# Optimization experiments

Measured on AMD Instinct MI355X. Metric: run time of the kernel, lower is better.

The kernel has to match this reference:

```python
import jax, jax.numpy as jnp
import numpy as np

H = 512        # hidden_dim
D_IN = 512     # input_dim
N_ACT = 16     # output_dim
DICT = 8192    # dict_len (episodic memory slots)
B = 4096       # batch
N_CYCLES = 10  # LCA iterations
DT_T = 0.6     # LCA dt/tau
EPS = 1e-8     # cosine-similarity eps


def setup_inputs() -> dict:
    key = jax.random.key(0)
    ks = jax.random.split(key, 12)
    NHT = 4 * H + 3  # (N_VSIG+1)*H + N_SSIG
    s = lambda i, shape, sc=1.0: jax.random.normal(ks[i], shape, jnp.float32) * sc
    return {
        "x_t": s(0, (1, B, D_IN)),
        "h_prev": s(1, (1, B, H), 0.1),
        "c_prev": s(2, (1, B, H), 0.1),
        "W_i2h": s(3, (NHT, D_IN), 1.0 / np.sqrt(D_IN)),
        "b_i2h": jnp.zeros((NHT,), jnp.float32),
        "W_h2h": s(4, (NHT, H), 1.0 / np.sqrt(H)),
        "b_h2h": jnp.zeros((NHT,), jnp.float32),
        "vals": s(5, (DICT, H), 0.1),  # episodic memory table
        "W_ih": s(6, (H, H), 1.0 / np.sqrt(H)),
        "b_ih": jnp.zeros((H,), jnp.float32),
        "W_actor": s(7, (N_ACT, H), 1.0 / np.sqrt(H)),
        "b_actor": jnp.zeros((N_ACT,), jnp.float32),
        "W_critic": s(8, (1, H), 1.0 / np.sqrt(H)),
        "b_critic": jnp.zeros((1,), jnp.float32),
        "mem_ptr": 0,
    }


def _lca(sim, leak, comp, w_input):
    # Leaky competing accumulator over memory slots; sim:[B,DICT], scalars:[B,1]
    ff = w_input * sim
    def step(V, _):
        inhib = comp * (jnp.sum(V, axis=-1, keepdims=True) - V)  # lateral inhibition (excl. self)
        V = jax.nn.relu(V + DT_T * (ff - leak * V - inhib))
        return V, None
    V, _ = jax.lax.scan(step, jnp.zeros_like(sim), None, length=N_CYCLES)
    return V


def reference(x_t, h_prev, c_prev, W_i2h, b_i2h, W_h2h, b_h2h, vals,
              W_ih, b_ih, W_actor, b_actor, W_critic, b_critic, mem_ptr):
    x, h, c = x_t[0], h_prev[0], c_prev[0]  # [B, dim]
    preact = x @ W_i2h.T + b_i2h + h @ W_h2h.T + b_h2h  # [B, 4H+3]
    gates = jax.nn.sigmoid(preact[:, :3 * H])
    f_t = gates[:, :H]
    o_t = gates[:, H:2 * H]
    i_t = gates[:, 2 * H:3 * H]
    inps = jax.nn.sigmoid(preact[:, 3 * H + 0])[:, None]  # input strength (gain=1)
    leak = jax.nn.sigmoid(preact[:, 3 * H + 1])[:, None]
    comp = jax.nn.sigmoid(preact[:, 3 * H + 2])[:, None]
    c_new = jnp.tanh(preact[:, 3 * H + 3:])
    c_t = c * f_t + i_t * c_new
    # --- recall: cosine similarity vs memory, then LCA competition ---
    qn = jnp.linalg.norm(c_t, axis=-1, keepdims=True)        # [B,1]
    mn = jnp.linalg.norm(vals, axis=-1, keepdims=True)       # [DICT,1]
    sim = (c_t @ vals.T) / jnp.maximum(qn * mn.T, EPS)       # [B,DICT]
    w = _lca(sim, leak, comp, inps)                          # [B,DICT]
    m_t = w @ vals                                           # [B,H]
    cm_t = c_t + m_t
    # --- encode: ring-buffer scatter write of cm_t into memory ---
    idx = (mem_ptr + jnp.arange(B)) % DICT
    new_vals = vals.at[idx].set(cm_t)
    h_t = o_t * jnp.tanh(cm_t)
    # --- A2C head ---
    a2c_h = jax.nn.relu(h_t @ W_ih.T + b_ih)
    pi = jax.nn.softmax(a2c_h @ W_actor.T + b_actor, axis=-1)
    value = a2c_h @ W_critic.T + b_critic
    return pi, value, h_t, cm_t, m_t, new_vals
```

## Files before the change

### kernel.cpp

```cpp
#include <hip/hip_runtime.h>
#include <hip/hip_fp16.h>
#include <math.h>

#define HH    512
#define DICT  8192
#define BATCH 4096
#define NCYC  10
#define DTT   0.6f

#define BM  128
#define BKT 64

using f16x8 = __attribute__((ext_vector_type(8))) _Float16;
using f32x4 = __attribute__((ext_vector_type(4))) float;

__device__ __forceinline__ float sigmoidf_(float x) { return 1.0f / (1.0f + __expf(-x)); }

__device__ __forceinline__ float waveReduceSum(float v) {
#pragma unroll
  for (int o = 1; o < 64; o <<= 1) v += __shfl_xor(v, o);
  return v;
}

__device__ __forceinline__ void gld16(const void* g, void* l) {
  __builtin_amdgcn_global_load_lds(
      (const __attribute__((address_space(1))) void*)g,
      (__attribute__((address_space(3))) void*)l, 16, 0, 0);
}

template<int N> __device__ __forceinline__ void vmwait() {
  if constexpr (N == 8)      asm volatile("s_waitcnt vmcnt(8)" ::: "memory");
  else if constexpr (N == 6) asm volatile("s_waitcnt vmcnt(6)" ::: "memory");
  else if constexpr (N == 2) asm volatile("s_waitcnt vmcnt(2)" ::: "memory");
  else                       asm volatile("s_waitcnt vmcnt(0)" ::: "memory");
  __builtin_amdgcn_sched_barrier(0);
}

__device__ __forceinline__ void blockbar() {
  asm volatile("" ::: "memory");
  __builtin_amdgcn_s_barrier();
  __builtin_amdgcn_sched_barrier(0);
}

template<int ROWS>
__device__ __forceinline__ void stage_tile(const __half* gbase, int ld, char* lds, int tid) {
  constexpr int ISS = ROWS * 8 / 256;
#pragma unroll
  for (int i = 0; i < ISS; ++i) {
    int cidx = i * 256 + tid;
    int row  = cidx >> 3;
    int slot = cidx & 7;
    int k4   = slot ^ (row & 7);
    gld16(gbase + (size_t)row * ld + k4 * 8, lds + cidx * 16);
  }
}

__device__ __forceinline__ f16x8 frag_ld(const char* lds, int row, int kchunk) {
  int slot = kchunk ^ (row & 7);
  return *(const f16x8*)(lds + row * 128 + slot * 16);
}

template<int FN>
__device__ __forceinline__ void tile_mfma(const char* As, const char* Bs,
                                          int lane, int wr, int wc, f32x4 (&acc)[4][FN]) {
  const int g = lane >> 4, r = lane & 15;
#pragma unroll
  for (int ks = 0; ks < 2; ++ks) {
    f16x8 af[4], bfr[FN];
#pragma unroll
    for (int i = 0; i < 4; ++i)
      af[i] = frag_ld(As, wr * 64 + i * 16 + r, ks * 4 + g);
#pragma unroll
    for (int j = 0; j < FN; ++j)
      bfr[j] = frag_ld(Bs, wc * (FN * 16) + j * 16 + r, ks * 4 + g);
#pragma unroll
    for (int i = 0; i < 4; ++i)
#pragma unroll
      for (int j = 0; j < FN; ++j)
        acc[i][j] = __builtin_amdgcn_mfma_f32_16x16x32_f16(af[i], bfr[j], acc[i][j], 0, 0, 0);
  }
}

template<int BN, int FN>
__device__ __forceinline__ void gemm_seg(const __half* A, int lda, const __half* B, int ldb,
                                         int m0, int n0, int K, char* lds, int tid,
                                         f32x4 (&acc)[4][FN]) {
  constexpr int ABYTES = BM * BKT * 2;
  constexpr int BBYTES = BN * BKT * 2;
  constexpr int BUF = ABYTES + BBYTES;
  constexpr int NL = (BM + BN) * 8 / 256;
  const int lane = tid & 63, wid = tid >> 6;
  const int wr = wid >> 1, wc = wid & 1;
  const int nt = K / BKT;
  const __half* Ab = A + (size_t)m0 * lda;
  const __half* Bb = B + (size_t)n0 * ldb;
  stage_tile<BM>(Ab, lda, lds, tid);
  stage_tile<BN>(Bb, ldb, lds + ABYTES, tid);
  int cur = 0;
  for (int t = 0; t < nt; ++t) {
    char* curb = lds + cur * BUF;
    if (t + 1 < nt) {
      char* nxt = lds + (cur ^ 1) * BUF;
      stage_tile<BM>(Ab + (t + 1) * BKT, lda, nxt, tid);
      stage_tile<BN>(Bb + (t + 1) * BKT, ldb, nxt + ABYTES, tid);
      vmwait<NL>();
    } else {
      vmwait<0>();
    }
    blockbar();
    tile_mfma<FN>(curb, curb + ABYTES, lane, wr, wc, acc);
    blockbar();
    cur ^= 1;
  }
}

__device__ __forceinline__ void zero_acc4(f32x4 (&a)[4][4]) {
  f32x4 z = {0.f, 0.f, 0.f, 0.f};
#pragma unroll
  for (int i = 0; i < 4; ++i)
#pragma unroll
    for (int j = 0; j < 4; ++j) a[i][j] = z;
}
__device__ __forceinline__ void zero_acc2(f32x4 (&a)[4][2]) {
  f32x4 z = {0.f, 0.f, 0.f, 0.f};
#pragma unroll
  for (int i = 0; i < 4; ++i)
#pragma unroll
    for (int j = 0; j < 2; ++j) a[i][j] = z;
}

__device__ __forceinline__ void stage_half(const __half* tilebase, int ld, char* ldstile,
                                           int h, int kcol, int tid) {
#pragma unroll
  for (int i = 0; i < 2; ++i) {
    int cidx = i * 512 + tid;
    int lrow = cidx >> 3;
    int slot = cidx & 7;
    int row  = h * 128 + lrow;
    int k4   = slot ^ (row & 7);
    gld16(tilebase + (size_t)row * ld + kcol + k4 * 8,
          ldstile + row * 128 + slot * 16);
  }
}

__device__ __forceinline__ f16x8 fragA8(const char* At, int fi, int wr, int ks, int lane) {
  int r = lane & 15, g = lane >> 4;
  int row = fi * 32 + wr * 16 + r;
  int slot = (ks * 4 + g) ^ (row & 7);
  return *(const f16x8*)(At + row * 128 + slot * 16);
}
__device__ __forceinline__ f16x8 fragB8(const char* Bt, int j, int wc, int ks, int lane) {
  int r = lane & 15, g = lane >> 4;
  int row = wc * 64 + j * 16 + r;
  int slot = (ks * 4 + g) ^ (row & 7);
  return *(const f16x8*)(Bt + row * 128 + slot * 16);
}

#define PHASE(TT, KS, MH, RB)                                                  \
  {                                                                            \
    if (RB) {                                                                  \
      _Pragma("unroll")                                                        \
      for (int j = 0; j < 4; ++j) bf[j] = fragB8((TT) + 32768, j, wc, KS, lane); \
    }                                                                          \
    f16x8 af[4];                                                               \
    _Pragma("unroll")                                                          \
    for (int i = 0; i < 4; ++i) af[i] = fragA8((TT), (MH)*4 + i, wr, KS, lane); \
    __builtin_amdgcn_s_setprio(1);                                             \
    _Pragma("unroll")                                                          \
    for (int i = 0; i < 4; ++i)                                                \
      _Pragma("unroll")                                                        \
      for (int j = 0; j < 4; ++j)                                              \
        acc[(MH)*4 + i][j] = __builtin_amdgcn_mfma_f32_16x16x32_f16(           \
            af[i], bf[j], acc[(MH)*4 + i][j], 0, 0, 0);                        \
    __builtin_amdgcn_s_setprio(0);                                             \
  }

template<int NT>
__device__ __forceinline__ void gemm_8ph(const __half* At, int lda,
                                         const __half* Bt, int ldb,
                                         char* lds, int tid, f32x4 (&acc)[8][4]) {
  const int lane = tid & 63, wid = tid >> 6;
  const int wr = wid >> 2, wc = wid & 3;
  char* b0 = lds;
  char* b1 = lds + 65536;
  stage_half(At, lda, b0, 0, 0, tid);
  stage_half(At, lda, b0, 1, 0, tid);
  stage_half(Bt, ldb, b0 + 32768, 0, 0, tid);
  stage_half(Bt, ldb, b0 + 32768, 1, 0, tid);
  stage_half(At, lda, b1, 0, 64, tid);
  constexpr int ITERS = NT / 2;
  f16x8 bf[4];
#pragma unroll 1
  for (int it = 0; it < ITERS; ++it) {
    const int kt = 2 * it;
    const bool stg = (it < ITERS - 1);
    vmwait<2>(); blockbar();
    stage_half(At, lda, b1, 1, (kt + 1) * 64, tid);
    PHASE(b0, 0, 0, true)
    blockbar();
    stage_half(Bt, ldb, b1 + 32768, 0, (kt + 1) * 64, tid);
    PHASE(b0, 0, 1, false)
    blockbar();
    stage_half(Bt, ldb, b1 + 32768, 1, (kt + 1) * 64, tid);
    PHASE(b0, 1, 0, true)
    blockbar();
    if (stg) stage_half(At, lda, b0, 0, (kt + 2) * 64, tid);
    PHASE(b0, 1, 1, false)
    if (stg) { vmwait<2>(); } else { vmwait<0>(); }
    blockbar();
    if (stg) stage_half(At, lda, b0, 1, (kt + 2) * 64, tid);
    PHASE(b1, 0, 0, true)
    blockbar();
    if (stg) stage_half(Bt, ldb, b0 + 32768, 0, (kt + 2) * 64, tid);
    PHASE(b1, 0, 1, false)
    blockbar();
    if (stg) stage_half(Bt, ldb, b0 + 32768, 1, (kt + 2) * 64, tid);
    PHASE(b1, 1, 0, true)
    blockbar();
    if (stg) stage_half(At, lda, b1, 0, (kt + 3) * 64, tid);
    PHASE(b1, 1, 1, false)
  }
}

__global__ __launch_bounds__(256) void k_prep(
    const float* __restrict__ x, const float* __restrict__ h,
    const float* __restrict__ Wi, const float* __restrict__ Wh, const float* __restrict__ Wih,
    const float* __restrict__ vals, const int* __restrict__ mptr,
    __half* __restrict__ x_h, __half* __restrict__ h_h,
    __half* __restrict__ Wip_h, __half* __restrict__ Whp_h, __half* __restrict__ Wih_h,
    float* __restrict__ nv, __half* __restrict__ vals_h, float* __restrict__ rmn,
    __half* __restrict__ vT) {
  __shared__ float tile[32][33];
  const int bid = blockIdx.x;
  if (bid < 6400) {
    int gq = bid * 256 + threadIdx.x;
    const float* src; __half* dst; int si, di;
    if (gq < 524288) {
      src = x; dst = x_h; si = di = gq * 4;
    } else if (gq < 1048576) {
      src = h; dst = h_h; si = di = (gq - 524288) * 4;
    } else if (gq < 1310720) {
      int iq = gq - 1048576;
      int jp = iq >> 7, k4 = (iq & 127) << 2;
      int U = jp >> 6, g = (jp >> 4) & 3, r = jp & 15;
      int u = U * 16 + r;
      int orig = g * 512 + u + (g == 3 ? 3 : 0);
      src = Wi; dst = Wip_h; si = orig * 512 + k4; di = jp * 512 + k4;
    } else if (gq < 1572864) {
      int iq = gq - 1310720;
      int jp = iq >> 7, k4 = (iq & 127) << 2;
      int U = jp >> 6, g = (jp >> 4) & 3, r = jp & 15;
      int u = U * 16 + r;
      int orig = g * 512 + u + (g == 3 ? 3 : 0);
      src = Wh; dst = Whp_h; si = orig * 512 + k4; di = jp * 512 + k4;
    } else if (gq < 1638400) {
      int iq = gq - 1572864;
      src = Wih; dst = Wih_h; si = di = iq * 4;
    } else return;
    float4 v = *(const float4*)(src + si);
    *(__half2*)(dst + di)     = __floats2half2_rn(v.x, v.y);
    *(__half2*)(dst + di + 2) = __floats2half2_rn(v.z, v.w);
  } else if (bid < 8448) {
    const int row  = (bid - 6400) * 4 + (threadIdx.x >> 6);
    const int lane = threadIdx.x & 63;
    const float* vr = vals + (size_t)row * HH + lane * 8;
    float4 a = *(const float4*)(vr);
    float4 b = *(const float4*)(vr + 4);
    if (((row + DICT - mptr[0]) & (DICT - 1)) >= BATCH) {
      float* nvp = nv + (size_t)row * HH + lane * 8;
      *(float4*)(nvp)     = a;
      *(float4*)(nvp + 4) = b;
    }
    __half* vh = vals_h + (size_t)row * HH + lane * 8;
    *(__half2*)(vh)     = __floats2half2_rn(a.x, a.y);
    *(__half2*)(vh + 2) = __floats2half2_rn(a.z, a.w);
    *(__half2*)(vh + 4) = __floats2half2_rn(b.x, b.y);
    *(__half2*)(vh + 6) = __floats2half2_rn(b.z, b.w);
    float ss = a.x * a.x + a.y * a.y + a.z * a.z + a.w * a.w
             + b.x * b.x + b.y * b.y + b.z * b.z + b.w * b.w;
    ss = waveReduceSum(ss);
    if (lane == 0) rmn[row] = 1.f / fmaxf(sqrtf(ss), 1e-12f);
  } else {
    const int idx = bid - 8448;
    const int r0 = (idx & 255) * 32, c0 = (idx >> 8) * 32;
    const int tr = threadIdx.x >> 5, tc = threadIdx.x & 31;
#pragma unroll
    for (int p = 0; p < 4; ++p)
      tile[tr + p * 8][tc] = vals[(size_t)(r0 + tr + p * 8) * HH + c0 + tc];
    __syncthreads();
#pragma unroll
    for (int p = 0; p < 4; ++p)
      vT[(size_t)(c0 + tr + p * 8) * DICT + r0 + tc] = __float2half(tile[tc][tr + p * 8]);
  }
}

__global__ __launch_bounds__(256) void k_preact(
    const __half* __restrict__ x_h, const __half* __restrict__ h_h,
    const __half* __restrict__ Wip, const __half* __restrict__ Whp,
    const float* __restrict__ bi, const float* __restrict__ bh,
    const float* __restrict__ c_prev,
    float* __restrict__ ct, float* __restrict__ ot, __half* __restrict__ ct_h) {
  __shared__ char smem[2 * (BM * BKT * 2 + 128 * BKT * 2)] __attribute__((aligned(16)));
  const int tid = threadIdx.x;
  const int m0 = blockIdx.y * 128, n0 = blockIdx.x * 128;
  f32x4 acc[4][4]; zero_acc4(acc);
  gemm_seg<128, 4>(x_h, HH, Wip, HH, m0, n0, HH, smem, tid, acc);
  gemm_seg<128, 4>(h_h, HH, Whp, HH, m0, n0, HH, smem, tid, acc);
  const int lane = tid & 63, wid = tid >> 6, wr = wid >> 1, wc = wid & 1;
  const int r = lane & 15;
  const int u = ((n0 >> 6) + wc) * 16 + r;
  float bsum[4];
#pragma unroll
  for (int g = 0; g < 4; ++g) {
    int orig = g * 512 + u + (g == 3 ? 3 : 0);
    bsum[g] = bi[orig] + bh[orig];
  }
#pragma unroll
  for (int fi = 0; fi < 4; ++fi)
#pragma unroll
    for (int q = 0; q < 4; ++q) {
      int m = m0 + wr * 64 + fi * 16 + (lane >> 4) * 4 + q;
      float f  = sigmoidf_(acc[fi][0][q] + bsum[0]);
      float o  = sigmoidf_(acc[fi][1][q] + bsum[1]);
      float ii = sigmoidf_(acc[fi][2][q] + bsum[2]);
      float cn = tanhf(acc[fi][3][q] + bsum[3]);
      size_t off = (size_t)m * HH + u;
      float cc = c_prev[off] * f + ii * cn;
      ct[off] = cc; ot[off] = o; ct_h[off] = __float2half(cc);
    }
}

__global__ __launch_bounds__(256) void k_scalars(
    const float* __restrict__ x, const float* __restrict__ h,
    const float* __restrict__ Wi, const float* __restrict__ Wh,
    const float* __restrict__ bi, const float* __restrict__ bh,
    const float* __restrict__ ct,
    float* __restrict__ inps, float* __restrict__ leak,
    float* __restrict__ comp, float* __restrict__ rqn) {
  const int b = blockIdx.x, wid = threadIdx.x >> 6, lane = threadIdx.x & 63;
  const int j = lane * 8;
  if (wid < 3) {
    const float* wi = Wi + (size_t)(1536 + wid) * HH + j;
    const float* wh = Wh + (size_t)(1536 + wid) * HH + j;
    const float* xr = x + (size_t)b * HH + j;
    const float* hr = h + (size_t)b * HH + j;
    float4 xa = *(const float4*)(xr), xb = *(const float4*)(xr + 4);
    float4 wa = *(const float4*)(wi), wb = *(const float4*)(wi + 4);
    float4 ha = *(const float4*)(hr), hb = *(const float4*)(hr + 4);
    float4 va = *(const float4*)(wh), vb = *(const float4*)(wh + 4);
    float s = xa.x * wa.x + xa.y * wa.y + xa.z * wa.z + xa.w * wa.w
            + xb.x * wb.x + xb.y * wb.y + xb.z * wb.z + xb.w * wb.w
            + ha.x * va.x + ha.y * va.y + ha.z * va.z + ha.w * va.w
            + hb.x * vb.x + hb.y * vb.y + hb.z * vb.z + hb.w * vb.w;
    s = waveReduceSum(s);
    if (lane == 0) {
      float v = sigmoidf_(s + bi[1536 + wid] + bh[1536 + wid]);
      if (wid == 0) inps[b] = v; else if (wid == 1) leak[b] = v; else comp[b] = v;
    }
  } else {
    const float* cr = ct + (size_t)b * HH + j;
    float4 a = *(const float4*)(cr), d = *(const float4*)(cr + 4);
    float ss = a.x * a.x + a.y * a.y + a.z * a.z + a.w * a.w
             + d.x * d.x + d.y * d.y + d.z * d.z + d.w * d.w;
    ss = waveReduceSum(ss);
    if (lane == 0) rqn[b] = 1.f / fmaxf(sqrtf(ss), 1e-12f);
  }
}

__global__ __launch_bounds__(512, 1) void k_sim(
    const __half* __restrict__ ct_h, const __half* __restrict__ vals_h,
    const float* __restrict__ rqn, const float* __restrict__ rmn,
    __half* __restrict__ sim_h) {
  extern __shared__ char dsm[];
  const int tid = threadIdx.x, lane = tid & 63, wid = tid >> 6;
  const int wr = wid >> 2, wc = wid & 3;
  const int bid = blockIdx.x;
  const int xcd = bid & 7, idx = bid >> 3;
  const int nt_ = xcd * 4 + (idx & 3);
  const int mt_ = idx >> 2;
  const int m0 = mt_ * 256, n0 = nt_ * 256;
  f32x4 acc[8][4];
  { f32x4 z = {0.f, 0.f, 0.f, 0.f};
#pragma unroll
    for (int i = 0; i < 8; ++i)
#pragma unroll
      for (int j = 0; j < 4; ++j) acc[i][j] = z; }
  gemm_8ph<8>(ct_h + (size_t)m0 * HH, HH, vals_h + (size_t)n0 * HH, HH, dsm, tid, acc);
  float* T = (float*)dsm;
  const int g = lane >> 4, r = lane & 15;
  const int lrow = tid >> 3;
  const int seg  = (tid & 7) * 16;
  float rmv0[16], rmv1[16];
#pragma unroll
  for (int k = 0; k < 4; ++k) {
    *(float4*)(rmv0 + k * 4) = *(const float4*)(rmn + n0 + seg + k * 4);
    *(float4*)(rmv1 + k * 4) = *(const float4*)(rmn + n0 + 128 + seg + k * 4);
  }
  __syncthreads();
#pragma unroll
  for (int p = 0; p < 4; ++p) {
    if (p) __syncthreads();
#pragma unroll
    for (int hf = 0; hf < 2; ++hf)
#pragma unroll
      for (int j = 0; j < 4; ++j)
#pragma unroll
        for (int q = 0; q < 4; ++q)
          T[(hf * 32 + wr * 16 + g * 4 + q) * 132 + wc * 64 + j * 16 + r] =
              acc[p * 2 + hf][j][q];
    __syncthreads();
    int m = m0 + p * 64 + lrow;
    float rq = rqn[m];
    const float* Tr = T + lrow * 132;
    f16x8 o0, o1;
#pragma unroll
    for (int j = 0; j < 8; ++j) o0[j] = (_Float16)(Tr[seg + j] * rq * rmv0[j]);
#pragma unroll
    for (int j = 0; j < 8; ++j) o1[j] = (_Float16)(Tr[seg + 8 + j] * rq * rmv0[8 + j]);
    *(f16x8*)(sim_h + (size_t)m * DICT + n0 + seg)     = o0;
    *(f16x8*)(sim_h + (size_t)m * DICT + n0 + seg + 8) = o1;
    f16x8 o2, o3;
#pragma unroll
    for (int j = 0; j < 8; ++j) o2[j] = (_Float16)(Tr[128 + seg + j] * rq * rmv1[j]);
#pragma unroll
    for (int j = 0; j < 8; ++j) o3[j] = (_Float16)(Tr[128 + seg + 8 + j] * rq * rmv1[8 + j]);
    *(f16x8*)(sim_h + (size_t)m * DICT + n0 + 128 + seg)     = o2;
    *(f16x8*)(sim_h + (size_t)m * DICT + n0 + 128 + seg + 8) = o3;
  }
}

__global__ __launch_bounds__(256) void k_lca(
    const __half* __restrict__ sim_h, const float* __restrict__ inps,
    const float* __restrict__ leak, const float* __restrict__ comp,
    __half* __restrict__ w_h) {
  const int b = blockIdx.x, t = threadIdx.x;
  const __half* srow = sim_h + (size_t)b * DICT + t * 32;
  const float ffs = DTT * inps[b];
  const float a   = 1.0f - DTT * leak[b] + DTT * comp[b];
  const float cdt = DTT * comp[b];
  float ff[32], V[32];
#pragma unroll
  for (int i = 0; i < 4; ++i) {
    f16x8 v8 = *(const f16x8*)(srow + i * 8);
#pragma unroll
    for (int j = 0; j < 8; ++j) { ff[i * 8 + j] = ffs * (float)v8[j]; V[i * 8 + j] = 0.f; }
  }
  __shared__ float ps[4];
  for (int it = 0; it < NCYC; ++it) {
    float s = 0.f;
#pragma unroll
    for (int i = 0; i < 32; ++i) s += V[i];
    s = waveReduceSum(s);
    if ((t & 63) == 0) ps[t >> 6] = s;
    __syncthreads();
    float S = ps[0] + ps[1] + ps[2] + ps[3];
    __syncthreads();
    float sub = cdt * S;
#pragma unroll
    for (int i = 0; i < 32; ++i) V[i] = fmaxf(fmaf(a, V[i], ff[i] - sub), 0.f);
  }
  __half* wrow = w_h + (size_t)b * DICT + t * 32;
#pragma unroll
  for (int i = 0; i < 4; ++i) {
    f16x8 o8;
#pragma unroll
    for (int j = 0; j < 8; ++j) o8[j] = (_Float16)V[i * 8 + j];
    *(f16x8*)(wrow + i * 8) = o8;
  }
}

__global__ __launch_bounds__(512, 1) void k_mt_p(
    const __half* __restrict__ w_h, const __half* __restrict__ vT_h,
    float* __restrict__ partial) {
  extern __shared__ char dsm[];
  const int tid = threadIdx.x, lane = tid & 63, wid = tid >> 6;
  const int wr = wid >> 2, wc = wid & 3;
  const int bid = blockIdx.x;
  const int s = bid & 7, idx = bid >> 3;
  const int n = idx & 1, m = idx >> 1;
  const int m0 = m * 256, n0 = n * 256;
  f32x4 acc[8][4];
  { f32x4 z = {0.f, 0.f, 0.f, 0.f};
#pragma unroll
    for (int i = 0; i < 8; ++i)
#pragma unroll
      for (int j = 0; j < 4; ++j) acc[i][j] = z; }
  gemm_8ph<16>(w_h + (size_t)m0 * DICT + s * 1024, DICT,
               vT_h + (size_t)n0 * DICT + s * 1024, DICT, dsm, tid, acc);
  float* T = (float*)dsm;
  const int g = lane >> 4, r = lane & 15;
  const int lrow = tid >> 3;
  const int seg  = (tid & 7) * 16;
  float* pbase = partial + (size_t)s * (BATCH * HH);
  __syncthreads();
#pragma unroll
  for (int p = 0; p < 4; ++p) {
    if (p) __syncthreads();
#pragma unroll
    for (int hf = 0; hf < 2; ++hf)
#pragma unroll
      for (int j = 0; j < 4; ++j)
#pragma unroll
        for (int q = 0; q < 4; ++q)
          T[(hf * 32 + wr * 16 + g * 4 + q) * 132 + wc * 64 + j * 16 + r] =
              acc[p * 2 + hf][j][q];
    __syncthreads();
    int mm = m0 + p * 64 + lrow;
    const float* Tr = T + lrow * 132;
    float* dst = pbase + (size_t)mm * HH + n0;
    *(float4*)(dst + seg)            = *(const float4*)(Tr + seg);
    *(float4*)(dst + seg + 4)        = *(const float4*)(Tr + seg + 4);
    *(float4*)(dst + seg + 8)        = *(const float4*)(Tr + seg + 8);
    *(float4*)(dst + seg + 12)       = *(const float4*)(Tr + seg + 12);
    *(float4*)(dst + 128 + seg)      = *(const float4*)(Tr + 128 + seg);
    *(float4*)(dst + 128 + seg + 4)  = *(const float4*)(Tr + 128 + seg + 4);
    *(float4*)(dst + 128 + seg + 8)  = *(const float4*)(Tr + 128 + seg + 8);
    *(float4*)(dst + 128 + seg + 12) = *(const float4*)(Tr + 128 + seg + 12);
  }
}

__global__ __launch_bounds__(256) void k_mt_red(
    const float* __restrict__ partial,
    const float* __restrict__ ct, const float* __restrict__ ot, const int* __restrict__ mptr,
    float* __restrict__ out_mt, float* __restrict__ out_cmt, float* __restrict__ out_ht,
    float* __restrict__ out_nv, __half* __restrict__ ht_h) {
  const int i4 = blockIdx.x * 256 + threadIdx.x;
  const size_t off = (size_t)i4 * 4;
  const int m = i4 >> 7;
  float4 p = *(const float4*)(partial + off);
#pragma unroll
  for (int s = 1; s < 8; ++s) {
    float4 q = *(const float4*)(partial + (size_t)s * 2097152 + off);
    p.x += q.x; p.y += q.y; p.z += q.z; p.w += q.w;
  }
  float4 c4 = *(const float4*)(ct + off);
  float4 o4 = *(const float4*)(ot + off);
  float4 cm, hv;
  cm.x = c4.x + p.x; hv.x = o4.x * tanhf(cm.x);
  cm.y = c4.y + p.y; hv.y = o4.y * tanhf(cm.y);
  cm.z = c4.z + p.z; hv.z = o4.z * tanhf(cm.z);
  cm.w = c4.w + p.w; hv.w = o4.w * tanhf(cm.w);
  *(float4*)(out_mt + off)  = p;
  *(float4*)(out_cmt + off) = cm;
  *(float4*)(out_ht + off)  = hv;
  *(__half2*)(ht_h + off)     = __floats2half2_rn(hv.x, hv.y);
  *(__half2*)(ht_h + off + 2) = __floats2half2_rn(hv.z, hv.w);
  const int nvrow = (mptr[0] + m) & (DICT - 1);
  *(float4*)(out_nv + (size_t)nvrow * HH + (off & 511)) = cm;
}

__global__ __launch_bounds__(256) void k_a2c(
    const __half* __restrict__ ht_h, const __half* __restrict__ Wih_h,
    const float* __restrict__ bih, float* __restrict__ a2c) {
  __shared__ char smem[2 * (BM * BKT * 2 + 64 * BKT * 2)] __attribute__((aligned(16)));
  const int tid = threadIdx.x;
  const int bid = blockIdx.x;
  const int xn = (bid >> 3) & 7, ym = (bid & 7) | ((bid >> 6) << 3);
  const int m0 = ym * 128, n0 = xn * 64;
  f32x4 acc[4][2]; zero_acc2(acc);
  gemm_seg<64, 2>(ht_h, HH, Wih_h, HH, m0, n0, HH, smem, tid, acc);
  const int lane = tid & 63, wid = tid >> 6, wr = wid >> 1, wc = wid & 1;
  float* T = (float*)smem;
  const int gg = lane >> 4, r = lane & 15;
  const int lrow = tid >> 3, c8 = (tid & 7) * 8;
  float4 b0 = *(const float4*)(bih + n0 + c8);
  float4 b1 = *(const float4*)(bih + n0 + c8 + 4);
#pragma unroll
  for (int fi = 0; fi < 4; ++fi) {
    if (fi) __syncthreads();
#pragma unroll
    for (int fj = 0; fj < 2; ++fj)
#pragma unroll
      for (int qq = 0; qq < 4; ++qq)
        T[(wr * 16 + gg * 4 + qq) * 68 + wc * 32 + fj * 16 + r] = acc[fi][fj][qq];
    __syncthreads();
    int mm = m0 + (lrow >> 4) * 64 + fi * 16 + (lrow & 15);
    float4 v0 = *(const float4*)(T + lrow * 68 + c8);
    float4 v1 = *(const float4*)(T + lrow * 68 + c8 + 4);
    v0.x = fmaxf(v0.x + b0.x, 0.f); v0.y = fmaxf(v0.y + b0.y, 0.f);
    v0.z = fmaxf(v0.z + b0.z, 0.f); v0.w = fmaxf(v0.w + b0.w, 0.f);
    v1.x = fmaxf(v1.x + b1.x, 0.f); v1.y = fmaxf(v1.y + b1.y, 0.f);
    v1.z = fmaxf(v1.z + b1.z, 0.f); v1.w = fmaxf(v1.w + b1.w, 0.f);
    float* dst = a2c + (size_t)mm * HH + n0 + c8;
    *(float4*)dst       = v0;
    *(float4*)(dst + 4) = v1;
  }
}

__global__ __launch_bounds__(256) void k_actor(
    const float* __restrict__ a2c,
    const float* __restrict__ Wact, const float* __restrict__ bact,
    const float* __restrict__ Wcr, const float* __restrict__ bcr,
    float* __restrict__ out_pi, float* __restrict__ out_val) {
  const int b = blockIdx.x * 4 + (threadIdx.x >> 6);
  const int lane = threadIdx.x & 63;
  const float* hrow = a2c + (size_t)b * HH;
  float4 a0 = *(const float4*)(hrow + (lane << 3));
  float4 a1 = *(const float4*)(hrow + (lane << 3) + 4);
  float lg[17];
#pragma unroll
  for (int o = 0; o < 17; ++o) {
    const float* wr = (o < 16) ? (Wact + (size_t)o * HH) : Wcr;
    float4 w0 = *(const float4*)(wr + (lane << 3));
    float4 w1 = *(const float4*)(wr + (lane << 3) + 4);
    float s = a0.x * w0.x + a0.y * w0.y + a0.z * w0.z + a0.w * w0.w
            + a1.x * w1.x + a1.y * w1.y + a1.z * w1.z + a1.w * w1.w;
    lg[o] = waveReduceSum(s);
  }
#pragma unroll
  for (int o = 0; o < 16; ++o) lg[o] += bact[o];
  float mx = lg[0];
#pragma unroll
  for (int o = 1; o < 16; ++o) mx = fmaxf(mx, lg[o]);
  float e[16], sum = 0.f;
#pragma unroll
  for (int o = 0; o < 16; ++o) { e[o] = __expf(lg[o] - mx); sum += e[o]; }
  float rs = 1.f / sum;
  if (lane == 0) {
#pragma unroll
    for (int o = 0; o < 16; ++o) out_pi[(size_t)b * 16 + o] = e[o] * rs;
    out_val[b] = lg[16] + bcr[0];
  }
}

extern "C" void kernel_launch(void* const* d_in, const int* in_sizes, int n_in,
                              void* d_out, int out_size, void* d_ws, size_t ws_size,
                              hipStream_t stream) {
  const float* x    = (const float*)d_in[0];
  const float* h    = (const float*)d_in[1];
  const float* c    = (const float*)d_in[2];
  const float* Wi   = (const float*)d_in[3];
  const float* bi   = (const float*)d_in[4];
  const float* Wh   = (const float*)d_in[5];
  const float* bh   = (const float*)d_in[6];
  const float* vals = (const float*)d_in[7];
  const float* Wih  = (const float*)d_in[8];
  const float* bih  = (const float*)d_in[9];
  const float* Wact = (const float*)d_in[10];
  const float* bact = (const float*)d_in[11];
  const float* Wcr  = (const float*)d_in[12];
  const float* bcr  = (const float*)d_in[13];
  const int*   mptr = (const int*)d_in[14];

  float* F = (float*)d_ws;
  __half* w_h    = (__half*)F;
  __half* sim_h   = (__half*)(F + 16777216);
  float*  a2c     = F + 16777216;
  float*  partial = F + 33554432;
  float*  ct     = F + 50331648;
  float*  ot     = F + 52428800;
  __half* ct_h   = (__half*)(F + 54525952);
  __half* vals_h = (__half*)(F + 55574528);
  __half* vT_h   = (__half*)(F + 57671680);
  __half* x_h    = (__half*)(F + 59768832);
  __half* ht_h   = x_h;
  __half* h_h    = (__half*)(F + 60817408);
  __half* Wip_h  = (__half*)(F + 61865984);
  __half* Whp_h  = (__half*)(F + 62423040);
  __half* Wih_h  = (__half*)(F + 62980096);
  float*  inps   = F + 63111168;
  float*  leak   = inps + 4096;
  float*  comp   = leak + 4096;
  float*  rqn    = comp + 4096;
  float*  rmn    = rqn + 4096;

  float* out     = (float*)d_out;
  float* out_pi  = out;
  float* out_val = out + 65536;
  float* out_ht  = out + 69632;
  float* out_cmt = out_ht + 2097152;
  float* out_mt  = out_cmt + 2097152;
  float* out_nv  = out_mt + 2097152;

  (void)hipFuncSetAttribute(reinterpret_cast<const void*>(k_sim),
                            hipFuncAttributeMaxDynamicSharedMemorySize, 131072);
  (void)hipFuncSetAttribute(reinterpret_cast<const void*>(k_mt_p),
                            hipFuncAttributeMaxDynamicSharedMemorySize, 131072);

  dim3 b256(256);
  dim3 b512(512);
  k_prep   <<<12544, b256, 0, stream>>>(x, h, Wi, Wh, Wih, vals, mptr,
                                        x_h, h_h, Wip_h, Whp_h, Wih_h,
                                        out_nv, vals_h, rmn, vT_h);
  k_preact <<<dim3(16, 32), b256, 0, stream>>>(x_h, h_h, Wip_h, Whp_h, bi, bh, c,
                                               ct, ot, ct_h);
  k_scalars<<<BATCH, b256, 0, stream>>>(x, h, Wi, Wh, bi, bh, ct, inps, leak, comp, rqn);
  k_sim    <<<512, b512, 131072, stream>>>(ct_h, vals_h, rqn, rmn, sim_h);
  k_lca    <<<BATCH, b256, 0, stream>>>(sim_h, inps, leak, comp, w_h);
  k_mt_p   <<<256, b512, 131072, stream>>>(w_h, vT_h, partial);
  k_mt_red <<<2048, b256, 0, stream>>>(partial, ct, ot, mptr,
                                       out_mt, out_cmt, out_ht, out_nv, ht_h);
  k_a2c    <<<256, b256, 0, stream>>>(ht_h, Wih_h, bih, a2c);
  k_actor  <<<BATCH / 4, b256, 0, stream>>>(a2c, Wact, bact, Wcr, bcr, out_pi, out_val);
}
```

Measured before the change: 237.0 us.

## Retile w@vals GEMM into smaller tiles with 4-way split-K and XCD-aware mapping

The m_t GEMM (B×DICT by DICT×H) changes from 256 blocks of 512 threads with 256x256 tiles and 8-way split-K to 1024 blocks of 256 threads with 128x64 tiles and 4-way split-K, using a static-shared gemm_seg helper. Block indices are remapped so that blocks sharing an XCD work on related tiles. The reduction kernel now sums 4 partials instead of 8, which halves the partial-buffer traffic. In exchange, the smaller tiles reuse each loaded operand less, so more A/B data is read from global memory.

```diff
diff --git a/kernel.cpp b/kernel.cpp
--- a/kernel.cpp
+++ b/kernel.cpp
@@ -469,53 +469,36 @@
   }
 }
 
-__global__ __launch_bounds__(512, 1) void k_mt_p(
+__global__ __launch_bounds__(256) void k_mt_p(
     const __half* __restrict__ w_h, const __half* __restrict__ vT_h,
     float* __restrict__ partial) {
-  extern __shared__ char dsm[];
-  const int tid = threadIdx.x, lane = tid & 63, wid = tid >> 6;
-  const int wr = wid >> 2, wc = wid & 3;
-  const int bid = blockIdx.x;
-  const int s = bid & 7, idx = bid >> 3;
-  const int n = idx & 1, m = idx >> 1;
-  const int m0 = m * 256, n0 = n * 256;
-  f32x4 acc[8][4];
-  { f32x4 z = {0.f, 0.f, 0.f, 0.f};
-#pragma unroll
-    for (int i = 0; i < 8; ++i)
-#pragma unroll
-      for (int j = 0; j < 4; ++j) acc[i][j] = z; }
-  gemm_8ph<16>(w_h + (size_t)m0 * DICT + s * 1024, DICT,
-               vT_h + (size_t)n0 * DICT + s * 1024, DICT, dsm, tid, acc);
-  float* T = (float*)dsm;
-  const int g = lane >> 4, r = lane & 15;
-  const int lrow = tid >> 3;
-  const int seg  = (tid & 7) * 16;
+  __shared__ char smem[2 * (BM * BKT * 2 + 64 * BKT * 2)] __attribute__((aligned(16)));
+  const int tid = threadIdx.x, bid = blockIdx.x;
+  const int xcd = bid & 7, idx = bid >> 3;
+  const int n = idx & 7, q = idx >> 3;
+  const int g = (q << 3) | xcd;
+  const int m = g >> 2, s = g & 3;
+  const int m0 = m * 128, n0 = n * 64;
+  f32x4 acc[4][2]; zero_acc2(acc);
+  gemm_seg<64, 2>(w_h + s * 2048, DICT, vT_h + s * 2048, DICT, m0, n0, 2048, smem, tid, acc);
+  const int lane = tid & 63, wid = tid >> 6, wr = wid >> 1, wc = wid & 1;
   float* pbase = partial + (size_t)s * (BATCH * HH);
-  __syncthreads();
-#pragma unroll
-  for (int p = 0; p < 4; ++p) {
-    if (p) __syncthreads();
-#pragma unroll
-    for (int hf = 0; hf < 2; ++hf)
-#pragma unroll
-      for (int j = 0; j < 4; ++j)
-#pragma unroll
-        for (int q = 0; q < 4; ++q)
-          T[(hf * 32 + wr * 16 + g * 4 + q) * 132 + wc * 64 + j * 16 + r] =
-              acc[p * 2 + hf][j][q];
+  float* T = (float*)smem;
+  const int gg = lane >> 4, r = lane & 15;
+  const int lrow = tid >> 3, c8 = (tid & 7) * 8;
+#pragma unroll
+  for (int fi = 0; fi < 4; ++fi) {
+    if (fi) __syncthreads();
+#pragma unroll
+    for (int fj = 0; fj < 2; ++fj)
+#pragma unroll
+      for (int qq = 0; qq < 4; ++qq)
+        T[(wr * 16 + gg * 4 + qq) * 68 + wc * 32 + fj * 16 + r] = acc[fi][fj][qq];
     __syncthreads();
-    int mm = m0 + p * 64 + lrow;
-    const float* Tr = T + lrow * 132;
-    float* dst = pbase + (size_t)mm * HH + n0;
-    *(float4*)(dst + seg)            = *(const float4*)(Tr + seg);
-    *(float4*)(dst + seg + 4)        = *(const float4*)(Tr + seg + 4);
-    *(float4*)(dst + seg + 8)        = *(const float4*)(Tr + seg + 8);
-    *(float4*)(dst + seg + 12)       = *(const float4*)(Tr + seg + 12);
-    *(float4*)(dst + 128 + seg)      = *(const float4*)(Tr + 128 + seg);
-    *(float4*)(dst + 128 + seg + 4)  = *(const float4*)(Tr + 128 + seg + 4);
-    *(float4*)(dst + 128 + seg + 8)  = *(const float4*)(Tr + 128 + seg + 8);
-    *(float4*)(dst + 128 + seg + 12) = *(const float4*)(Tr + 128 + seg + 12);
+    int mm = m0 + (lrow >> 4) * 64 + fi * 16 + (lrow & 15);
+    float* dst = pbase + (size_t)mm * HH + n0 + c8;
+    *(float4*)dst       = *(const float4*)(T + lrow * 68 + c8);
+    *(float4*)(dst + 4) = *(const float4*)(T + lrow * 68 + c8 + 4);
   }
 }
 
@@ -527,12 +510,14 @@
   const int i4 = blockIdx.x * 256 + threadIdx.x;
   const size_t off = (size_t)i4 * 4;
   const int m = i4 >> 7;
-  float4 p = *(const float4*)(partial + off);
-#pragma unroll
-  for (int s = 1; s < 8; ++s) {
-    float4 q = *(const float4*)(partial + (size_t)s * 2097152 + off);
-    p.x += q.x; p.y += q.y; p.z += q.z; p.w += q.w;
-  }
+  float4 p  = *(const float4*)(partial + off);
+  float4 p1 = *(const float4*)(partial + 2097152 + off);
+  float4 p2 = *(const float4*)(partial + 4194304 + off);
+  float4 p3 = *(const float4*)(partial + 6291456 + off);
+  p.x += p1.x + p2.x + p3.x;
+  p.y += p1.y + p2.y + p3.y;
+  p.z += p1.z + p2.z + p3.z;
+  p.w += p1.w + p2.w + p3.w;
   float4 c4 = *(const float4*)(ct + off);
   float4 o4 = *(const float4*)(ot + off);
   float4 cm, hv;
@@ -674,8 +659,6 @@
 
   (void)hipFuncSetAttribute(reinterpret_cast<const void*>(k_sim),
                             hipFuncAttributeMaxDynamicSharedMemorySize, 131072);
-  (void)hipFuncSetAttribute(reinterpret_cast<const void*>(k_mt_p),
-                            hipFuncAttributeMaxDynamicSharedMemorySize, 131072);
 
   dim3 b256(256);
   dim3 b512(512);
@@ -687,7 +670,7 @@
   k_scalars<<<BATCH, b256, 0, stream>>>(x, h, Wi, Wh, bi, bh, ct, inps, leak, comp, rqn);
   k_sim    <<<512, b512, 131072, stream>>>(ct_h, vals_h, rqn, rmn, sim_h);
   k_lca    <<<BATCH, b256, 0, stream>>>(sim_h, inps, leak, comp, w_h);
-  k_mt_p   <<<256, b512, 131072, stream>>>(w_h, vT_h, partial);
+  k_mt_p   <<<1024, b256, 0, stream>>>(w_h, vT_h, partial);
   k_mt_red <<<2048, b256, 0, stream>>>(partial, ct, ot, mptr,
                                        out_mt, out_cmt, out_ht, out_nv, ht_h);
   k_a2c    <<<256, b256, 0, stream>>>(ht_h, Wih_h, bih, a2c);
```

After: 222.4 us. 1.07x faster.
